# Kernel tuning notes

Measured on AMD Instinct MI355X. Metric: run time of the kernel, lower is better.

The kernel has to match this reference:

```python
import jax, jax.numpy as jnp
import numpy as np
import math

E, H, FFN, NQ = 1024, 16, 4096, 8
B, T = 2, 2048
EPS = 1e-5

def layernorm(x, g, b):
    mu = jnp.mean(x, axis=-1, keepdims=True)
    var = jnp.mean(jnp.square(x - mu), axis=-1, keepdims=True)
    return (x - mu) * jax.lax.rsqrt(var + EPS) * g + b

def setup_inputs() -> dict:
    key = jax.random.key(0)
    ks = jax.random.split(key, 8)
    x = jax.random.normal(ks[0], (B, T, E), dtype=jnp.float32)
    mask = jnp.ones((B, T, T), dtype=bool)
    # constant quantum measurement output: PauliZ expectations of a fixed
    # RandomLayer circuit applied to |0..0> (independent of the input tokens)
    q_out = jax.random.uniform(ks[1], (NQ,), minval=-1.0, maxval=1.0, dtype=jnp.float32)
    s1 = 1.0 / math.sqrt(NQ)
    w1 = jax.random.uniform(ks[2], (NQ, FFN), minval=-s1, maxval=s1, dtype=jnp.float32)
    b1 = jnp.zeros((FFN,), dtype=jnp.float32)
    s2 = 1.0 / math.sqrt(FFN)
    w2 = jax.random.uniform(ks[3], (FFN, E), minval=-s2, maxval=s2, dtype=jnp.float32)
    b2 = jnp.zeros((E,), dtype=jnp.float32)
    g1 = jnp.ones((E,), dtype=jnp.float32); be1 = jnp.zeros((E,), dtype=jnp.float32)
    g2 = jnp.ones((E,), dtype=jnp.float32); be2 = jnp.zeros((E,), dtype=jnp.float32)
    return dict(x=x, mask=mask, q_out=q_out, w1=w1, b1=b1, w2=w2, b2=b2,
                g1=g1, be1=be1, g2=g2, be2=be2)

def reference(x, mask, q_out, w1, b1, w2, b2, g1, be1, g2, be2):
    b, t, e = x.shape
    d_k = e // H
    # q = k = v = head-split x (module has no QKV projections)
    q = x.reshape(b, t, H, d_k).transpose(0, 2, 1, 3)  # [B,H,T,d_k]
    scores = jnp.einsum('bhqd,bhkd->bhqk', q, q) / math.sqrt(d_k)
    scores = jnp.where(mask[:, None, :, :], scores, -1e9)
    attn = jax.nn.softmax(scores, axis=-1)
    out = jnp.einsum('bhqk,bhkd->bhqd', attn, q)
    attn_out = out.transpose(0, 2, 1, 3).reshape(b, t, e)
    x1 = layernorm(x + attn_out, g1, be1)
    # quantum FFN: constant measurement vector broadcast over all tokens
    h = jnp.broadcast_to(q_out, (b, t, NQ))
    h = jnp.dot(h, w1) + b1
    ffn_out = jnp.dot(jax.nn.relu(h), w2) + b2
    return layernorm(x1 + ffn_out, g2, be2)
```

## Files before the change

### kernel.cpp

```cpp
#include <hip/hip_runtime.h>

#define E_   1024
#define H_   16
#define DK_  64
#define FFN_ 4096
#define NQ_  8
#define B_   2
#define T_   2048
#define QBLK 128
#define KVBLK 64
#define NT_  (T_ / KVBLK)

#define NPART 256
#define ROWS_PER_PART (FFN_ / NPART)

typedef __attribute__((ext_vector_type(8))) __bf16 bf16x8;
typedef __attribute__((ext_vector_type(4))) float f32x4;

__device__ __forceinline__ __bf16 tobf(float f) { return (__bf16)f; }

__device__ __forceinline__ unsigned pk2(float a, float b) {
  union { __bf16 h; unsigned short u; } ua, ub;
  ua.h = (__bf16)a; ub.h = (__bf16)b;
  return (unsigned)ua.u | ((unsigned)ub.u << 16);
}

__global__ __launch_bounds__(256)
void cvt_kernel(const float* __restrict__ x, __bf16* __restrict__ xbf) {
  const size_t base = ((size_t)blockIdx.x * 256 + threadIdx.x) * 8;
  float4 a = *reinterpret_cast<const float4*>(x + base);
  float4 b = *reinterpret_cast<const float4*>(x + base + 4);
  bf16x8 v;
  v[0] = tobf(a.x); v[1] = tobf(a.y); v[2] = tobf(a.z); v[3] = tobf(a.w);
  v[4] = tobf(b.x); v[5] = tobf(b.y); v[6] = tobf(b.z); v[7] = tobf(b.w);
  *reinterpret_cast<bf16x8*>(xbf + base) = v;
}

__global__ __launch_bounds__(256)
void ffn_part_kernel(const float* __restrict__ q_out, const float* __restrict__ w1,
                     const float* __restrict__ b1, const float* __restrict__ w2,
                     float* __restrict__ part) {
  __shared__ float h[ROWS_PER_PART];
  const int tid = threadIdx.x;
  const int p = blockIdx.x;
  const int f0 = p * ROWS_PER_PART;
  if (tid < ROWS_PER_PART) {
    const int f = f0 + tid;
    float a = b1[f];
#pragma unroll
    for (int n = 0; n < NQ_; ++n) a += q_out[n] * w1[n * FFN_ + f];
    h[tid] = fmaxf(a, 0.f);
  }
  __syncthreads();
  float4 acc = {0.f, 0.f, 0.f, 0.f};
#pragma unroll
  for (int j = 0; j < ROWS_PER_PART; ++j) {
    const float hf = h[j];
    float4 w = reinterpret_cast<const float4*>(w2 + (size_t)(f0 + j) * E_)[tid];
    acc.x += hf * w.x; acc.y += hf * w.y; acc.z += hf * w.z; acc.w += hf * w.w;
  }
  reinterpret_cast<float4*>(part + (size_t)p * E_)[tid] = acc;
}

__global__ __launch_bounds__(256)
void ffn_reduce_kernel(const float* __restrict__ part, const float* __restrict__ b2,
                       float* __restrict__ ffn_c) {
  const int e = blockIdx.x * 256 + threadIdx.x;
  float a = b2[e];
  for (int r = 0; r < NPART; ++r) a += part[(size_t)r * E_ + e];
  ffn_c[e] = a;
}

__global__ __launch_bounds__(256)
void attn_kernel(const __bf16* __restrict__ xbf, float* __restrict__ out) {
  __shared__ __bf16 Kt[2][KVBLK][DK_ + 8];
  __shared__ __bf16 VtF[2][DK_ * KVBLK];
  __shared__ __bf16 Pl[4][32][DK_ + 8];

  const int tid  = threadIdx.x;
  const int wave = tid >> 6;
  const int lane = tid & 63;
  const int l16  = lane & 15;
  const int lhi  = lane >> 4;

  const int bh = blockIdx.y;
  const int b  = bh >> 4;
  const int h  = bh & 15;
  const int qbase = blockIdx.x * QBLK;
  const __bf16* xb = xbf + (size_t)b * T_ * E_ + h * DK_;

  bf16x8 qa[2][2];
  {
    const __bf16 sc = (__bf16)0.125f;
#pragma unroll
    for (int g = 0; g < 2; ++g) {
      const __bf16* qrow = xb + (size_t)(qbase + wave * 32 + g * 16 + l16) * E_;
      bf16x8 v0 = *reinterpret_cast<const bf16x8*>(qrow + lhi * 8);
      bf16x8 v1 = *reinterpret_cast<const bf16x8*>(qrow + 32 + lhi * 8);
#pragma unroll
      for (int j = 0; j < 8; ++j) { v0[j] *= sc; v1[j] *= sc; }
      qa[g][0] = v0; qa[g][1] = v1;
    }
  }

  f32x4 acc[2][4];
#pragma unroll
  for (int g = 0; g < 2; ++g)
#pragma unroll
    for (int td = 0; td < 4; ++td) acc[g][td] = (f32x4){0.f, 0.f, 0.f, 0.f};
  float lg0 = 0.f, lg1 = 0.f;

  const int kp = tid >> 3;
  const int d0 = (tid & 7) * 8;
  const __bf16* kvbase = xb + (size_t)(2 * kp) * E_ + d0;

  {
    uint4 p0 = *reinterpret_cast<const uint4*>(kvbase);
    uint4 p1 = *reinterpret_cast<const uint4*>(kvbase + E_);
    *reinterpret_cast<uint4*>(&Kt[0][2 * kp][d0])     = p0;
    *reinterpret_cast<uint4*>(&Kt[0][2 * kp + 1][d0]) = p1;
    union U4 { uint4 v; unsigned short s[8]; } u0, u1;
    u0.v = p0; u1.v = p1;
#pragma unroll
    for (int j = 0; j < 8; ++j) {
      const int d = d0 + j;
      const unsigned w = (unsigned)u0.s[j] | ((unsigned)u1.s[j] << 16);
      const int byte = d * 128 + ((4 * kp) ^ ((((d & 7) ^ ((d >> 3) & 7))) << 4));
      *reinterpret_cast<unsigned*>(reinterpret_cast<char*>(&VtF[0][0]) + byte) = w;
    }
  }
  __syncthreads();

  for (int t = 0; t < NT_; ++t) {
    const int cur = t & 1;
    const __bf16* Ktc = &Kt[cur][0][0];
    const char*   Vtc = reinterpret_cast<const char*>(&VtF[cur][0]);

    uint4 nr0, nr1;
    const bool have_next = (t + 1 < NT_);
    if (have_next) {
      const __bf16* nb = kvbase + (size_t)(t + 1) * KVBLK * E_;
      nr0 = *reinterpret_cast<const uint4*>(nb);
      nr1 = *reinterpret_cast<const uint4*>(nb + E_);
    }

    f32x4 s0[4], s1[4];
    __builtin_amdgcn_s_setprio(1);
#pragma unroll
    for (int tn = 0; tn < 4; ++tn) {
      const __bf16* kr = Ktc + (tn * 16 + l16) * (DK_ + 8);
      bf16x8 ka0 = *reinterpret_cast<const bf16x8*>(kr + lhi * 8);
      bf16x8 ka1 = *reinterpret_cast<const bf16x8*>(kr + 32 + lhi * 8);
      f32x4 c0 = (f32x4){0.f, 0.f, 0.f, 0.f};
      c0 = __builtin_amdgcn_mfma_f32_16x16x32_bf16(ka0, qa[0][0], c0, 0, 0, 0);
      c0 = __builtin_amdgcn_mfma_f32_16x16x32_bf16(ka1, qa[0][1], c0, 0, 0, 0);
      s0[tn] = c0;
      f32x4 c1 = (f32x4){0.f, 0.f, 0.f, 0.f};
      c1 = __builtin_amdgcn_mfma_f32_16x16x32_bf16(ka0, qa[1][0], c1, 0, 0, 0);
      c1 = __builtin_amdgcn_mfma_f32_16x16x32_bf16(ka1, qa[1][1], c1, 0, 0, 0);
      s1[tn] = c1;
    }
    __builtin_amdgcn_s_setprio(0);

#pragma unroll
    for (int tn = 0; tn < 4; ++tn) {
      float p0 = __expf(s0[tn][0]), p1 = __expf(s0[tn][1]);
      float p2 = __expf(s0[tn][2]), p3 = __expf(s0[tn][3]);
      lg0 += (p0 + p1) + (p2 + p3);
      uint2 w; w.x = pk2(p0, p1); w.y = pk2(p2, p3);
      *reinterpret_cast<uint2*>(&Pl[wave][l16][tn * 16 + lhi * 4]) = w;
      float q0 = __expf(s1[tn][0]), q1 = __expf(s1[tn][1]);
      float q2 = __expf(s1[tn][2]), q3 = __expf(s1[tn][3]);
      lg1 += (q0 + q1) + (q2 + q3);
      uint2 u; u.x = pk2(q0, q1); u.y = pk2(q2, q3);
      *reinterpret_cast<uint2*>(&Pl[wave][16 + l16][tn * 16 + lhi * 4]) = u;
    }
    asm volatile("s_waitcnt lgkmcnt(0)" ::: "memory");

    __builtin_amdgcn_s_setprio(1);
#pragma unroll
    for (int kb = 0; kb < 2; ++kb) {
      bf16x8 pa0 = *reinterpret_cast<const bf16x8*>(&Pl[wave][l16][kb * 32 + lhi * 8]);
      bf16x8 pa1 = *reinterpret_cast<const bf16x8*>(&Pl[wave][16 + l16][kb * 32 + lhi * 8]);
#pragma unroll
      for (int td = 0; td < 4; ++td) {
        const int d = td * 16 + l16;
        const int byte = d * 128 +
                         ((kb * 64 + lhi * 16) ^ (((d & 7) ^ ((d >> 3) & 7)) << 4));
        bf16x8 vv = *reinterpret_cast<const bf16x8*>(Vtc + byte);
        acc[0][td] = __builtin_amdgcn_mfma_f32_16x16x32_bf16(pa0, vv, acc[0][td], 0, 0, 0);
        acc[1][td] = __builtin_amdgcn_mfma_f32_16x16x32_bf16(pa1, vv, acc[1][td], 0, 0, 0);
      }
    }
    __builtin_amdgcn_s_setprio(0);

    if (have_next) {
      const int nxt = cur ^ 1;
      *reinterpret_cast<uint4*>(&Kt[nxt][2 * kp][d0])     = nr0;
      *reinterpret_cast<uint4*>(&Kt[nxt][2 * kp + 1][d0]) = nr1;
      union U4 { uint4 v; unsigned short s[8]; } u0, u1;
      u0.v = nr0; u1.v = nr1;
      char* vb = reinterpret_cast<char*>(&VtF[nxt][0]);
#pragma unroll
      for (int j = 0; j < 8; ++j) {
        const int d = d0 + j;
        const unsigned w = (unsigned)u0.s[j] | ((unsigned)u1.s[j] << 16);
        const int byte = d * 128 + ((4 * kp) ^ ((((d & 7) ^ ((d >> 3) & 7))) << 4));
        *reinterpret_cast<unsigned*>(vb + byte) = w;
      }
    }
    __syncthreads();
  }

  lg0 += __shfl_xor(lg0, 16); lg0 += __shfl_xor(lg0, 32);
  lg1 += __shfl_xor(lg1, 16); lg1 += __shfl_xor(lg1, 32);
  float inv0[4], inv1[4];
#pragma unroll
  for (int i = 0; i < 4; ++i) {
    inv0[i] = 1.f / __shfl(lg0, lhi * 4 + i);
    inv1[i] = 1.f / __shfl(lg1, lhi * 4 + i);
  }
#pragma unroll
  for (int td = 0; td < 4; ++td)
#pragma unroll
    for (int i = 0; i < 4; ++i) {
      const int col = h * DK_ + td * 16 + l16;
      const size_t r0 = (size_t)b * T_ + qbase + wave * 32 + lhi * 4 + i;
      out[r0 * E_ + col]        = acc[0][td][i] * inv0[i];
      out[(r0 + 16) * E_ + col] = acc[1][td][i] * inv1[i];
    }
}

__device__ __forceinline__ float block_sum(float v, float* redrow, int lane, int wave) {
#pragma unroll
  for (int off = 1; off < 64; off <<= 1) v += __shfl_xor(v, off);
  if (lane == 0) redrow[wave] = v;
  __syncthreads();
  return redrow[0] + redrow[1] + redrow[2] + redrow[3];
}

__global__ __launch_bounds__(256)
void ln_kernel(const float* __restrict__ x, const float* __restrict__ ffn_c,
               const float* __restrict__ g1, const float* __restrict__ be1,
               const float* __restrict__ g2, const float* __restrict__ be2,
               float* io) {
  __shared__ float red[4][4];
  const int row = blockIdx.x;
  const int tid = threadIdx.x;
  const int lane = tid & 63, wave = tid >> 6;
  const float* xr = x + (size_t)row * E_;
  float* ior = io + (size_t)row * E_;

  float4 xv = reinterpret_cast<const float4*>(xr)[tid];
  float4 av = reinterpret_cast<const float4*>(ior)[tid];
  float v[4] = {xv.x + av.x, xv.y + av.y, xv.z + av.z, xv.w + av.w};

  float mu1 = block_sum(v[0] + v[1] + v[2] + v[3], red[0], lane, wave) * (1.f / E_);
  float q1 = 0.f;
#pragma unroll
  for (int j = 0; j < 4; ++j) { float d = v[j] - mu1; q1 += d * d; }
  float var1 = block_sum(q1, red[1], lane, wave) * (1.f / E_);
  float rs1 = rsqrtf(var1 + 1e-5f);

  const int e0 = tid * 4;
  float y[4];
#pragma unroll
  for (int j = 0; j < 4; ++j)
    y[j] = (v[j] - mu1) * rs1 * g1[e0 + j] + be1[e0 + j] + ffn_c[e0 + j];

  float mu2 = block_sum(y[0] + y[1] + y[2] + y[3], red[2], lane, wave) * (1.f / E_);
  float q2 = 0.f;
#pragma unroll
  for (int j = 0; j < 4; ++j) { float d = y[j] - mu2; q2 += d * d; }
  float var2 = block_sum(q2, red[3], lane, wave) * (1.f / E_);
  float rs2 = rsqrtf(var2 + 1e-5f);

  float4 o;
  o.x = (y[0] - mu2) * rs2 * g2[e0 + 0] + be2[e0 + 0];
  o.y = (y[1] - mu2) * rs2 * g2[e0 + 1] + be2[e0 + 1];
  o.z = (y[2] - mu2) * rs2 * g2[e0 + 2] + be2[e0 + 2];
  o.w = (y[3] - mu2) * rs2 * g2[e0 + 3] + be2[e0 + 3];
  reinterpret_cast<float4*>(ior)[tid] = o;
}

extern "C" void kernel_launch(void* const* d_in, const int* in_sizes, int n_in,
                              void* d_out, int out_size, void* d_ws, size_t ws_size,
                              hipStream_t stream) {
  (void)in_sizes; (void)n_in; (void)out_size; (void)ws_size;
  const float* x     = (const float*)d_in[0];
  const float* q_out = (const float*)d_in[2];
  const float* w1    = (const float*)d_in[3];
  const float* b1    = (const float*)d_in[4];
  const float* w2    = (const float*)d_in[5];
  const float* b2    = (const float*)d_in[6];
  const float* g1    = (const float*)d_in[7];
  const float* be1   = (const float*)d_in[8];
  const float* g2    = (const float*)d_in[9];
  const float* be2   = (const float*)d_in[10];
  float* out   = (float*)d_out;
  float* ffn_c = (float*)d_ws;
  float* part  = (float*)d_ws + E_;
  __bf16* xbf  = (__bf16*)((float*)d_ws + E_ + NPART * E_);

  cvt_kernel<<<(B_ * T_ * E_) / (256 * 8), 256, 0, stream>>>(x, xbf);
  ffn_part_kernel<<<NPART, 256, 0, stream>>>(q_out, w1, b1, w2, part);
  ffn_reduce_kernel<<<E_ / 256, 256, 0, stream>>>(part, b2, ffn_c);
  dim3 ag(T_ / QBLK, B_ * H_);
  attn_kernel<<<ag, 256, 0, stream>>>(xbf, out);
  ln_kernel<<<B_ * T_, 256, 0, stream>>>(x, ffn_c, g1, be1, g2, be2, out);
}
```

Before: 94.56 us.

## Split attention over KV halves and merge partial sums in layernorm

Adds a split-K dimension to the attention grid so each block handles half of the key/value sequence. Unnormalized partial outputs and row sums go to workspace, and the layernorm kernel merges and normalizes them. This doubles the block count from 512 to 1024 to fill more of the GPU. The P scratch buffer now reuses the idle next K buffer to cut shared memory, at the cost of extra serialization and extra global traffic for the second partial output. Correctness relies on the softmax having no max subtraction, so partial exp-sums can simply be added.

```diff
diff --git a/kernel.cpp b/kernel.cpp
--- a/kernel.cpp
+++ b/kernel.cpp
@@ -9,7 +9,8 @@
 #define T_   2048
 #define QBLK 128
 #define KVBLK 64
-#define NT_  (T_ / KVBLK)
+#define KSPLIT 2
+#define NTS  (T_ / KVBLK / KSPLIT)
 
 #define NPART 256
 #define ROWS_PER_PART (FFN_ / NPART)
@@ -72,10 +73,11 @@
 }
 
 __global__ __launch_bounds__(256)
-void attn_kernel(const __bf16* __restrict__ xbf, float* __restrict__ out) {
+void attn_kernel(const __bf16* __restrict__ xbf, float* __restrict__ On0,
+                 float* __restrict__ On1, float* __restrict__ lb0,
+                 float* __restrict__ lb1) {
   __shared__ __bf16 Kt[2][KVBLK][DK_ + 8];
   __shared__ __bf16 VtF[2][DK_ * KVBLK];
-  __shared__ __bf16 Pl[4][32][DK_ + 8];
 
   const int tid  = threadIdx.x;
   const int wave = tid >> 6;
@@ -86,6 +88,7 @@
   const int bh = blockIdx.y;
   const int b  = bh >> 4;
   const int h  = bh & 15;
+  const int ks = blockIdx.z;
   const int qbase = blockIdx.x * QBLK;
   const __bf16* xb = xbf + (size_t)b * T_ * E_ + h * DK_;
 
@@ -112,7 +115,7 @@
 
   const int kp = tid >> 3;
   const int d0 = (tid & 7) * 8;
-  const __bf16* kvbase = xb + (size_t)(2 * kp) * E_ + d0;
+  const __bf16* kvbase = xb + (size_t)(ks * (T_ / KSPLIT) + 2 * kp) * E_ + d0;
 
   {
     uint4 p0 = *reinterpret_cast<const uint4*>(kvbase);
@@ -131,13 +134,15 @@
   }
   __syncthreads();
 
-  for (int t = 0; t < NT_; ++t) {
+  for (int t = 0; t < NTS; ++t) {
     const int cur = t & 1;
+    const int nxt = cur ^ 1;
     const __bf16* Ktc = &Kt[cur][0][0];
     const char*   Vtc = reinterpret_cast<const char*>(&VtF[cur][0]);
+    __bf16* Plw = &Kt[nxt][wave * 16][0];
 
     uint4 nr0, nr1;
-    const bool have_next = (t + 1 < NT_);
+    const bool have_next = (t + 1 < NTS);
     if (have_next) {
       const __bf16* nb = kvbase + (size_t)(t + 1) * KVBLK * E_;
       nr0 = *reinterpret_cast<const uint4*>(nb);
@@ -168,34 +173,43 @@
       float p2 = __expf(s0[tn][2]), p3 = __expf(s0[tn][3]);
       lg0 += (p0 + p1) + (p2 + p3);
       uint2 w; w.x = pk2(p0, p1); w.y = pk2(p2, p3);
-      *reinterpret_cast<uint2*>(&Pl[wave][l16][tn * 16 + lhi * 4]) = w;
-      float q0 = __expf(s1[tn][0]), q1 = __expf(s1[tn][1]);
-      float q2 = __expf(s1[tn][2]), q3 = __expf(s1[tn][3]);
-      lg1 += (q0 + q1) + (q2 + q3);
-      uint2 u; u.x = pk2(q0, q1); u.y = pk2(q2, q3);
-      *reinterpret_cast<uint2*>(&Pl[wave][16 + l16][tn * 16 + lhi * 4]) = u;
+      *reinterpret_cast<uint2*>(Plw + l16 * (DK_ + 8) + tn * 16 + lhi * 4) = w;
     }
     asm volatile("s_waitcnt lgkmcnt(0)" ::: "memory");
+    bf16x8 pa0[2], pa1[2];
+    pa0[0] = *reinterpret_cast<const bf16x8*>(Plw + l16 * (DK_ + 8) + lhi * 8);
+    pa0[1] = *reinterpret_cast<const bf16x8*>(Plw + l16 * (DK_ + 8) + 32 + lhi * 8);
+    asm volatile("s_waitcnt lgkmcnt(0)" ::: "memory");
+
+#pragma unroll
+    for (int tn = 0; tn < 4; ++tn) {
+      float p0 = __expf(s1[tn][0]), p1 = __expf(s1[tn][1]);
+      float p2 = __expf(s1[tn][2]), p3 = __expf(s1[tn][3]);
+      lg1 += (p0 + p1) + (p2 + p3);
+      uint2 w; w.x = pk2(p0, p1); w.y = pk2(p2, p3);
+      *reinterpret_cast<uint2*>(Plw + l16 * (DK_ + 8) + tn * 16 + lhi * 4) = w;
+    }
+    asm volatile("s_waitcnt lgkmcnt(0)" ::: "memory");
+    pa1[0] = *reinterpret_cast<const bf16x8*>(Plw + l16 * (DK_ + 8) + lhi * 8);
+    pa1[1] = *reinterpret_cast<const bf16x8*>(Plw + l16 * (DK_ + 8) + 32 + lhi * 8);
 
     __builtin_amdgcn_s_setprio(1);
 #pragma unroll
     for (int kb = 0; kb < 2; ++kb) {
-      bf16x8 pa0 = *reinterpret_cast<const bf16x8*>(&Pl[wave][l16][kb * 32 + lhi * 8]);
-      bf16x8 pa1 = *reinterpret_cast<const bf16x8*>(&Pl[wave][16 + l16][kb * 32 + lhi * 8]);
 #pragma unroll
       for (int td = 0; td < 4; ++td) {
         const int d = td * 16 + l16;
         const int byte = d * 128 +
                          ((kb * 64 + lhi * 16) ^ (((d & 7) ^ ((d >> 3) & 7)) << 4));
         bf16x8 vv = *reinterpret_cast<const bf16x8*>(Vtc + byte);
-        acc[0][td] = __builtin_amdgcn_mfma_f32_16x16x32_bf16(pa0, vv, acc[0][td], 0, 0, 0);
-        acc[1][td] = __builtin_amdgcn_mfma_f32_16x16x32_bf16(pa1, vv, acc[1][td], 0, 0, 0);
+        acc[0][td] = __builtin_amdgcn_mfma_f32_16x16x32_bf16(pa0[kb], vv, acc[0][td], 0, 0, 0);
+        acc[1][td] = __builtin_amdgcn_mfma_f32_16x16x32_bf16(pa1[kb], vv, acc[1][td], 0, 0, 0);
       }
     }
     __builtin_amdgcn_s_setprio(0);
 
+    asm volatile("s_waitcnt lgkmcnt(0)" ::: "memory");
     if (have_next) {
-      const int nxt = cur ^ 1;
       *reinterpret_cast<uint4*>(&Kt[nxt][2 * kp][d0])     = nr0;
       *reinterpret_cast<uint4*>(&Kt[nxt][2 * kp + 1][d0]) = nr1;
       union U4 { uint4 v; unsigned short s[8]; } u0, u1;
@@ -214,11 +228,11 @@
 
   lg0 += __shfl_xor(lg0, 16); lg0 += __shfl_xor(lg0, 32);
   lg1 += __shfl_xor(lg1, 16); lg1 += __shfl_xor(lg1, 32);
-  float inv0[4], inv1[4];
-#pragma unroll
-  for (int i = 0; i < 4; ++i) {
-    inv0[i] = 1.f / __shfl(lg0, lhi * 4 + i);
-    inv1[i] = 1.f / __shfl(lg1, lhi * 4 + i);
+  float* On = ks ? On1 : On0;
+  float* lb = ks ? lb1 : lb0;
+  if (lhi == 0) {
+    lb[(size_t)bh * T_ + qbase + wave * 32 + l16]      = lg0;
+    lb[(size_t)bh * T_ + qbase + wave * 32 + 16 + l16] = lg1;
   }
 #pragma unroll
   for (int td = 0; td < 4; ++td)
@@ -226,8 +240,8 @@
     for (int i = 0; i < 4; ++i) {
       const int col = h * DK_ + td * 16 + l16;
       const size_t r0 = (size_t)b * T_ + qbase + wave * 32 + lhi * 4 + i;
-      out[r0 * E_ + col]        = acc[0][td][i] * inv0[i];
-      out[(r0 + 16) * E_ + col] = acc[1][td][i] * inv1[i];
+      On[r0 * E_ + col]        = acc[0][td][i];
+      On[(r0 + 16) * E_ + col] = acc[1][td][i];
     }
 }
 
@@ -240,7 +254,9 @@
 }
 
 __global__ __launch_bounds__(256)
-void ln_kernel(const float* __restrict__ x, const float* __restrict__ ffn_c,
+void ln_kernel(const float* __restrict__ x, const float* __restrict__ On2,
+               const float* __restrict__ lb0, const float* __restrict__ lb1,
+               const float* __restrict__ ffn_c,
                const float* __restrict__ g1, const float* __restrict__ be1,
                const float* __restrict__ g2, const float* __restrict__ be2,
                float* io) {
@@ -248,12 +264,22 @@
   const int row = blockIdx.x;
   const int tid = threadIdx.x;
   const int lane = tid & 63, wave = tid >> 6;
+  const int bq = row;
+  const int b = bq >> 11;
+  const int q = bq & (T_ - 1);
   const float* xr = x + (size_t)row * E_;
   float* ior = io + (size_t)row * E_;
 
+  const int e0 = tid * 4;
+  const int h = e0 >> 6;
+  const size_t lidx = ((size_t)(b * H_ + h)) * T_ + q;
+  const float invl = 1.f / (lb0[lidx] + lb1[lidx]);
+
   float4 xv = reinterpret_cast<const float4*>(xr)[tid];
-  float4 av = reinterpret_cast<const float4*>(ior)[tid];
-  float v[4] = {xv.x + av.x, xv.y + av.y, xv.z + av.z, xv.w + av.w};
+  float4 a1 = reinterpret_cast<const float4*>(ior)[tid];
+  float4 a2 = reinterpret_cast<const float4*>(On2 + (size_t)row * E_)[tid];
+  float v[4] = {xv.x + (a1.x + a2.x) * invl, xv.y + (a1.y + a2.y) * invl,
+                xv.z + (a1.z + a2.z) * invl, xv.w + (a1.w + a2.w) * invl};
 
   float mu1 = block_sum(v[0] + v[1] + v[2] + v[3], red[0], lane, wave) * (1.f / E_);
   float q1 = 0.f;
@@ -262,7 +288,6 @@
   float var1 = block_sum(q1, red[1], lane, wave) * (1.f / E_);
   float rs1 = rsqrtf(var1 + 1e-5f);
 
-  const int e0 = tid * 4;
   float y[4];
 #pragma unroll
   for (int j = 0; j < 4; ++j)
@@ -298,14 +323,18 @@
   const float* g2    = (const float*)d_in[9];
   const float* be2   = (const float*)d_in[10];
   float* out   = (float*)d_out;
+
   float* ffn_c = (float*)d_ws;
-  float* part  = (float*)d_ws + E_;
-  __bf16* xbf  = (__bf16*)((float*)d_ws + E_ + NPART * E_);
+  float* part  = ffn_c + E_;
+  __bf16* xbf  = (__bf16*)(part + (size_t)NPART * E_);
+  float* On2   = (float*)((char*)xbf + (size_t)B_ * T_ * E_ * 2);
+  float* lb0   = On2 + (size_t)B_ * T_ * E_;
+  float* lb1   = lb0 + (size_t)B_ * H_ * T_;
 
   cvt_kernel<<<(B_ * T_ * E_) / (256 * 8), 256, 0, stream>>>(x, xbf);
   ffn_part_kernel<<<NPART, 256, 0, stream>>>(q_out, w1, b1, w2, part);
   ffn_reduce_kernel<<<E_ / 256, 256, 0, stream>>>(part, b2, ffn_c);
-  dim3 ag(T_ / QBLK, B_ * H_);
-  attn_kernel<<<ag, 256, 0, stream>>>(xbf, out);
-  ln_kernel<<<B_ * T_, 256, 0, stream>>>(x, ffn_c, g1, be1, g2, be2, out);
-}
+  dim3 ag(T_ / QBLK, B_ * H_, KSPLIT);
+  attn_kernel<<<ag, 256, 0, stream>>>(xbf, out, On2, lb0, lb1);
+  ln_kernel<<<B_ * T_, 256, 0, stream>>>(x, On2, lb0, lb1, ffn_c, g1, be1, g2, be2, out);
+}
```

New measurement: 97.91 us. +3.5%, slower.

## Pre-transpose V in conversion kernel to replace scattered LDS writes in attention

Applied to the files above, without the earlier changes.

The bf16 conversion kernel now also writes a per-head transposed copy of x (d-major over tokens), staged through a shared-memory tile. The attention kernel loads V from this transposed buffer and stores it to the swizzled LDS layout with two 16-byte writes per thread, replacing eight scattered 4-byte writes plus the shuffling. This lowers LDS store and ALU work in the inner loop. In exchange it costs extra global writes and reads for the second copy, and the conversion kernel gains a shared-memory transpose that may have bank conflicts.

```diff
diff --git a/kernel.cpp b/kernel.cpp
--- a/kernel.cpp
+++ b/kernel.cpp
@@ -26,14 +26,43 @@
 }
 
 __global__ __launch_bounds__(256)
-void cvt_kernel(const float* __restrict__ x, __bf16* __restrict__ xbf) {
-  const size_t base = ((size_t)blockIdx.x * 256 + threadIdx.x) * 8;
-  float4 a = *reinterpret_cast<const float4*>(x + base);
-  float4 b = *reinterpret_cast<const float4*>(x + base + 4);
-  bf16x8 v;
-  v[0] = tobf(a.x); v[1] = tobf(a.y); v[2] = tobf(a.z); v[3] = tobf(a.w);
-  v[4] = tobf(b.x); v[5] = tobf(b.y); v[6] = tobf(b.z); v[7] = tobf(b.w);
-  *reinterpret_cast<bf16x8*>(xbf + base) = v;
+void cvt_kernel(const float* __restrict__ x, __bf16* __restrict__ xbf,
+                __bf16* __restrict__ xbfT) {
+  __shared__ __bf16 tile[64][66];
+  const int tid = threadIdx.x;
+  const int bid = blockIdx.x;
+  const int h  = bid & 15;
+  const int tt = (bid >> 4) & 31;
+  const int b  = bid >> 9;
+  const float* src = x + ((size_t)(b * T_ + tt * 64)) * E_ + h * 64;
+
+#pragma unroll
+  for (int u = 0; u < 2; ++u) {
+    const int idx = tid + 256 * u;
+    const int r = idx >> 3;
+    const int c = (idx & 7) * 8;
+    float4 f0 = *reinterpret_cast<const float4*>(src + (size_t)r * E_ + c);
+    float4 f1 = *reinterpret_cast<const float4*>(src + (size_t)r * E_ + c + 4);
+    bf16x8 v;
+    v[0] = tobf(f0.x); v[1] = tobf(f0.y); v[2] = tobf(f0.z); v[3] = tobf(f0.w);
+    v[4] = tobf(f1.x); v[5] = tobf(f1.y); v[6] = tobf(f1.z); v[7] = tobf(f1.w);
+    *reinterpret_cast<bf16x8*>(
+        &xbf[((size_t)(b * T_ + tt * 64 + r)) * E_ + h * 64 + c]) = v;
+#pragma unroll
+    for (int j = 0; j < 8; ++j) tile[r][c + j] = v[j];
+  }
+  __syncthreads();
+#pragma unroll
+  for (int u = 0; u < 2; ++u) {
+    const int idx = tid + 256 * u;
+    const int d  = idx >> 3;
+    const int tc = (idx & 7) * 8;
+    bf16x8 v;
+#pragma unroll
+    for (int j = 0; j < 8; ++j) v[j] = tile[tc + j][d];
+    *reinterpret_cast<bf16x8*>(
+        &xbfT[((size_t)((b * H_ + h) * DK_ + d)) * T_ + tt * 64 + tc]) = v;
+  }
 }
 
 __global__ __launch_bounds__(256)
@@ -72,7 +101,8 @@
 }
 
 __global__ __launch_bounds__(256)
-void attn_kernel(const __bf16* __restrict__ xbf, float* __restrict__ out) {
+void attn_kernel(const __bf16* __restrict__ xbf, const __bf16* __restrict__ xbfT,
+                 float* __restrict__ out) {
   __shared__ __bf16 Kt[2][KVBLK][DK_ + 8];
   __shared__ __bf16 VtF[2][DK_ * KVBLK];
   __shared__ __bf16 Pl[4][32][DK_ + 8];
@@ -112,22 +142,27 @@
 
   const int kp = tid >> 3;
   const int d0 = (tid & 7) * 8;
-  const __bf16* kvbase = xb + (size_t)(2 * kp) * E_ + d0;
+  const __bf16* kbase = xb + (size_t)(2 * kp) * E_ + d0;
+  const int dv = tid >> 3;
+  const int kv = (tid & 7) * 8;
+  const __bf16* vbase = xbfT + ((size_t)(bh * DK_ + dv)) * T_ + kv;
+
+  const int rotA = ((dv & 7) ^ ((dv >> 3) & 7)) << 4;
+  const int dvB = dv + 32;
+  const int rotB = ((dvB & 7) ^ ((dvB >> 3) & 7)) << 4;
+  const int vbyteA = dv * 128 + ((kv * 2) ^ rotA);
+  const int vbyteB = dvB * 128 + ((kv * 2) ^ rotB);
 
   {
-    uint4 p0 = *reinterpret_cast<const uint4*>(kvbase);
-    uint4 p1 = *reinterpret_cast<const uint4*>(kvbase + E_);
-    *reinterpret_cast<uint4*>(&Kt[0][2 * kp][d0])     = p0;
-    *reinterpret_cast<uint4*>(&Kt[0][2 * kp + 1][d0]) = p1;
-    union U4 { uint4 v; unsigned short s[8]; } u0, u1;
-    u0.v = p0; u1.v = p1;
-#pragma unroll
-    for (int j = 0; j < 8; ++j) {
-      const int d = d0 + j;
-      const unsigned w = (unsigned)u0.s[j] | ((unsigned)u1.s[j] << 16);
-      const int byte = d * 128 + ((4 * kp) ^ ((((d & 7) ^ ((d >> 3) & 7))) << 4));
-      *reinterpret_cast<unsigned*>(reinterpret_cast<char*>(&VtF[0][0]) + byte) = w;
-    }
+    uint4 k0 = *reinterpret_cast<const uint4*>(kbase);
+    uint4 k1 = *reinterpret_cast<const uint4*>(kbase + E_);
+    uint4 v0 = *reinterpret_cast<const uint4*>(vbase);
+    uint4 v1 = *reinterpret_cast<const uint4*>(vbase + (size_t)32 * T_);
+    *reinterpret_cast<uint4*>(&Kt[0][2 * kp][d0])     = k0;
+    *reinterpret_cast<uint4*>(&Kt[0][2 * kp + 1][d0]) = k1;
+    char* vb = reinterpret_cast<char*>(&VtF[0][0]);
+    *reinterpret_cast<uint4*>(vb + vbyteA) = v0;
+    *reinterpret_cast<uint4*>(vb + vbyteB) = v1;
   }
   __syncthreads();
 
@@ -136,12 +171,15 @@
     const __bf16* Ktc = &Kt[cur][0][0];
     const char*   Vtc = reinterpret_cast<const char*>(&VtF[cur][0]);
 
-    uint4 nr0, nr1;
+    uint4 nk0, nk1, nv0, nv1;
     const bool have_next = (t + 1 < NT_);
     if (have_next) {
-      const __bf16* nb = kvbase + (size_t)(t + 1) * KVBLK * E_;
-      nr0 = *reinterpret_cast<const uint4*>(nb);
-      nr1 = *reinterpret_cast<const uint4*>(nb + E_);
+      const __bf16* nk = kbase + (size_t)(t + 1) * KVBLK * E_;
+      const __bf16* nv = vbase + (size_t)(t + 1) * KVBLK;
+      nk0 = *reinterpret_cast<const uint4*>(nk);
+      nk1 = *reinterpret_cast<const uint4*>(nk + E_);
+      nv0 = *reinterpret_cast<const uint4*>(nv);
+      nv1 = *reinterpret_cast<const uint4*>(nv + (size_t)32 * T_);
     }
 
     f32x4 s0[4], s1[4];
@@ -196,18 +234,11 @@
 
     if (have_next) {
       const int nxt = cur ^ 1;
-      *reinterpret_cast<uint4*>(&Kt[nxt][2 * kp][d0])     = nr0;
-      *reinterpret_cast<uint4*>(&Kt[nxt][2 * kp + 1][d0]) = nr1;
-      union U4 { uint4 v; unsigned short s[8]; } u0, u1;
-      u0.v = nr0; u1.v = nr1;
+      *reinterpret_cast<uint4*>(&Kt[nxt][2 * kp][d0])     = nk0;
+      *reinterpret_cast<uint4*>(&Kt[nxt][2 * kp + 1][d0]) = nk1;
       char* vb = reinterpret_cast<char*>(&VtF[nxt][0]);
-#pragma unroll
-      for (int j = 0; j < 8; ++j) {
-        const int d = d0 + j;
-        const unsigned w = (unsigned)u0.s[j] | ((unsigned)u1.s[j] << 16);
-        const int byte = d * 128 + ((4 * kp) ^ ((((d & 7) ^ ((d >> 3) & 7))) << 4));
-        *reinterpret_cast<unsigned*>(vb + byte) = w;
-      }
+      *reinterpret_cast<uint4*>(vb + vbyteA) = nv0;
+      *reinterpret_cast<uint4*>(vb + vbyteB) = nv1;
     }
     __syncthreads();
   }
@@ -298,14 +329,16 @@
   const float* g2    = (const float*)d_in[9];
   const float* be2   = (const float*)d_in[10];
   float* out   = (float*)d_out;
+
   float* ffn_c = (float*)d_ws;
-  float* part  = (float*)d_ws + E_;
-  __bf16* xbf  = (__bf16*)((float*)d_ws + E_ + NPART * E_);
-
-  cvt_kernel<<<(B_ * T_ * E_) / (256 * 8), 256, 0, stream>>>(x, xbf);
+  float* part  = ffn_c + E_;
+  __bf16* xbf  = (__bf16*)(part + (size_t)NPART * E_);
+  __bf16* xbfT = xbf + (size_t)B_ * T_ * E_;
+
+  cvt_kernel<<<B_ * (T_ / 64) * H_, 256, 0, stream>>>(x, xbf, xbfT);
   ffn_part_kernel<<<NPART, 256, 0, stream>>>(q_out, w1, b1, w2, part);
   ffn_reduce_kernel<<<E_ / 256, 256, 0, stream>>>(part, b2, ffn_c);
   dim3 ag(T_ / QBLK, B_ * H_);
-  attn_kernel<<<ag, 256, 0, stream>>>(xbf, out);
+  attn_kernel<<<ag, 256, 0, stream>>>(xbf, xbfT, out);
   ln_kernel<<<B_ * T_, 256, 0, stream>>>(x, ffn_c, g1, be1, g2, be2, out);
 }
```

After: 92.04 us. 2.7% less time.
